# Optimization experiments

Hardware: AMD Instinct MI355X
Metric: run time of the kernel (lower is better)

The kernel has to match this reference:

```python
import jax, jax.numpy as jnp
import numpy as np

NUM_NODES = 100000
NUM_EDGES = 400000
F_IN = 16          # num_node_features
F_EDGE = 8         # num_edge_features
EMB = 16           # emb_size
NUM_GRAPHS = 256


def setup_inputs() -> dict:
    key = jax.random.key(0)
    ks = jax.random.split(key, 12)
    x = jax.random.normal(ks[0], (NUM_NODES, F_IN), dtype=jnp.float32)
    edge_index = jax.random.randint(ks[1], (2, NUM_EDGES), 0, NUM_NODES, dtype=jnp.int32)
    edge_attr = jax.random.normal(ks[2], (NUM_EDGES, F_EDGE), dtype=jnp.float32)
    batch = jnp.sort(jax.random.randint(ks[3], (NUM_NODES,), 0, NUM_GRAPHS, dtype=jnp.int32))
    s = 0.1
    # edge-network MLP: Linear(F_EDGE -> F_IN*EMB) + ReLU (torch Linear convention: W[out,in])
    nn1_w = jax.random.normal(ks[4], (F_IN * EMB, F_EDGE), dtype=jnp.float32) * s
    nn1_b = jax.random.normal(ks[5], (F_IN * EMB,), dtype=jnp.float32) * s
    # NNConv root weight (bias=False Linear) + separate bias
    root_w = jax.random.normal(ks[6], (EMB, F_IN), dtype=jnp.float32) * s
    conv_b = jax.random.normal(ks[7], (EMB,), dtype=jnp.float32) * s
    lin1_w = jax.random.normal(ks[8], (EMB, 2 * EMB), dtype=jnp.float32) * s
    lin1_b = jax.random.normal(ks[9], (EMB,), dtype=jnp.float32) * s
    lin2_w = jax.random.normal(ks[10], (1, EMB), dtype=jnp.float32) * s
    lin2_b = jax.random.normal(ks[11], (1,), dtype=jnp.float32) * s
    return {"x": x, "edge_index": edge_index, "edge_attr": edge_attr, "batch": batch,
            "nn1_w": nn1_w, "nn1_b": nn1_b, "root_w": root_w, "conv_b": conv_b,
            "lin1_w": lin1_w, "lin1_b": lin1_b, "lin2_w": lin2_w, "lin2_b": lin2_b}


def reference(x, edge_index, edge_attr, batch, nn1_w, nn1_b, root_w, conv_b,
              lin1_w, lin1_b, lin2_w, lin2_b):
    N = x.shape[0]
    src, dst = edge_index[0], edge_index[1]  # PyG: message flows src(j) -> dst(i)
    # edge network -> per-edge weight matrices [E, F_IN, EMB]
    w = jax.nn.relu(edge_attr @ nn1_w.T + nn1_b).reshape(-1, F_IN, EMB)
    # gather source features, per-edge matmul
    msg = jnp.einsum('ei,eio->eo', x[src], w)  # [E, EMB]
    # scatter-mean into target nodes
    sums = jax.ops.segment_sum(msg, dst, num_segments=N)
    cnt = jax.ops.segment_sum(jnp.ones((msg.shape[0],), msg.dtype), dst, num_segments=N)
    agg = sums / jnp.maximum(cnt, 1.0)[:, None]
    # NNConv: root transform + aggregated messages + bias, then outer ReLU
    h = jax.nn.relu(agg + x @ root_w.T + conv_b)  # [N, EMB]
    # global max pool and global mean pool per graph
    gmax = jax.ops.segment_max(h, batch, num_segments=NUM_GRAPHS)
    gsum = jax.ops.segment_sum(h, batch, num_segments=NUM_GRAPHS)
    gcnt = jax.ops.segment_sum(jnp.ones((N,), h.dtype), batch, num_segments=NUM_GRAPHS)
    gmean = gsum / jnp.maximum(gcnt, 1.0)[:, None]
    pooled = jnp.concatenate([gmax, gmean], axis=1)  # [G, 2*EMB]
    h2 = jax.nn.relu(pooled @ lin1_w.T + lin1_b)
    out = h2 @ lin2_w.T + lin2_b  # [G, 1]
    return out
```

## Files before the change

kernel.cpp:

```cpp
#include <hip/hip_runtime.h>

#define NUM_NODES 100000
#define NUM_EDGES 400000
#define F_IN 16
#define F_EDGE 8
#define EMB 16
#define NUM_GRAPHS 256

#define EDGE_GRID 2048
#define NTILES (NUM_EDGES / 64)

#define NPB 128
#define NODE_BLOCKS ((NUM_NODES + NPB - 1) / NPB)

#define WS_ZERO_FLOATS (NUM_NODES * EMB + NUM_NODES + 2 * NUM_GRAPHS * EMB + NUM_GRAPHS)

__global__ __launch_bounds__(256) void zero_kernel(float4* __restrict__ ws)
{
    const int n4 = WS_ZERO_FLOATS / 4;
    const int stride = gridDim.x * 256;
    for (int i = blockIdx.x * 256 + threadIdx.x; i < n4; i += stride)
        ws[i] = make_float4(0.f, 0.f, 0.f, 0.f);
}

__global__ __launch_bounds__(256) void edge_kernel(
    const float* __restrict__ x, const int* __restrict__ ei,
    const float* __restrict__ ea, const float* __restrict__ nn1_w,
    const float* __restrict__ nn1_b, float* __restrict__ sums,
    float* __restrict__ cnt)
{
    __shared__ float wtp[256 * 12];

    const int tid = threadIdx.x;
    const int eL  = tid >> 4;
    const int o   = tid & 15;

    #pragma unroll
    for (int t = tid; t < F_IN * EMB * F_EDGE; t += 256)
        wtp[(t >> 3) * 12 + (t & 7)] = nn1_w[t];
    wtp[tid * 12 + 8] = nn1_b[tid];
    __syncthreads();

    float br[F_IN];
    #pragma unroll
    for (int i = 0; i < F_IN; i++) br[i] = wtp[(i * 16 + o) * 12 + 8];

    for (int t = blockIdx.x; t < NTILES; t += EDGE_GRID) {
        const int e0 = t * 64 + eL * 4;

        const int4 s4 = *(const int4*)&ei[e0];
        const int4 d4 = *(const int4*)&ei[NUM_EDGES + e0];
        const int src[4] = {s4.x, s4.y, s4.z, s4.w};
        const int dst[4] = {d4.x, d4.y, d4.z, d4.w};

        float4 A[8];
        #pragma unroll
        for (int r = 0; r < 8; r++) A[r] = *(const float4*)&ea[e0 * 8 + 4 * r];

        float acc[4] = {0.f, 0.f, 0.f, 0.f};

        #pragma unroll
        for (int h = 0; h < 2; h++) {
            float4 xa[4], xb[4];
            #pragma unroll
            for (int e = 0; e < 4; e++) {
                xa[e] = *(const float4*)&x[src[e] * 16 + h * 8];
                xb[e] = *(const float4*)&x[src[e] * 16 + h * 8 + 4];
            }
            #pragma unroll
            for (int ii = 0; ii < 8; ii++) {
                const int i = h * 8 + ii;
                const float* wr = &wtp[(i * 16 + o) * 12];
                const float4 w0 = *(const float4*)wr;
                const float4 w1 = *(const float4*)(wr + 4);
                #pragma unroll
                for (int e = 0; e < 4; e++) {
                    const float4 a0 = A[2 * e];
                    const float4 a1 = A[2 * e + 1];
                    float u = br[i];
                    u = fmaf(a0.x, w0.x, u); u = fmaf(a0.y, w0.y, u);
                    u = fmaf(a0.z, w0.z, u); u = fmaf(a0.w, w0.w, u);
                    u = fmaf(a1.x, w1.x, u); u = fmaf(a1.y, w1.y, u);
                    u = fmaf(a1.z, w1.z, u); u = fmaf(a1.w, w1.w, u);
                    const float xv = (ii < 4)
                        ? ((ii == 0) ? xa[e].x : (ii == 1) ? xa[e].y
                                     : (ii == 2) ? xa[e].z : xa[e].w)
                        : ((ii == 4) ? xb[e].x : (ii == 5) ? xb[e].y
                                     : (ii == 6) ? xb[e].z : xb[e].w);
                    acc[e] = fmaf(xv, fmaxf(u, 0.f), acc[e]);
                }
            }
        }

        #pragma unroll
        for (int e = 0; e < 4; e++)
            atomicAdd(&sums[dst[e] * 16 + o], acc[e]);
        if (o == 0) {
            #pragma unroll
            for (int e = 0; e < 4; e++)
                atomicAdd(&cnt[dst[e]], 1.f);
        }
    }
}

__global__ __launch_bounds__(256) void node_kernel(
    const float* __restrict__ x, const int* __restrict__ batch,
    const float* __restrict__ root_w, const float* __restrict__ conv_b,
    const float* __restrict__ sums, const float* __restrict__ cnt,
    unsigned int* __restrict__ gmax, float* __restrict__ gsum,
    float* __restrict__ gcnt)
{
    __shared__ float rwT[256];
    __shared__ float xsh[256];
    __shared__ float ssh[256];
    __shared__ float csh[16];
    __shared__ int   bsh[16];
    __shared__ float hsh[256];

    const int tid = threadIdx.x;
    const int j   = tid >> 4;
    const int o   = tid & 15;
    const int n0  = blockIdx.x * NPB;

    rwT[(tid & 15) * 16 + (tid >> 4)] = root_w[tid];
    const float cb = conv_b[o];

    int   curg = batch[n0];
    float am = 0.f, asum = 0.f, ac = 0.f;

    for (int s0 = 0; s0 < NPB; s0 += 16) {
        const int base = n0 + s0;
        const int idx  = base * 16 + tid;
        const bool v   = (idx < NUM_NODES * 16);
        const float xv = v ? x[idx]    : 0.f;
        const float sv = v ? sums[idx] : 0.f;
        float cv = 1.f; int bv = -1;
        if (tid < 16) {
            const int n = base + tid;
            if (n < NUM_NODES) { cv = cnt[n]; bv = batch[n]; }
        }
        __syncthreads();
        xsh[tid] = xv; ssh[tid] = sv;
        if (tid < 16) { csh[tid] = cv; bsh[tid] = bv; }
        __syncthreads();

        float a = cb + ssh[j * 16 + o] / fmaxf(csh[j], 1.f);
        #pragma unroll
        for (int i = 0; i < F_IN; i++)
            a = fmaf(xsh[j * 16 + i], rwT[i * 16 + o], a);
        hsh[tid] = fmaxf(a, 0.f);
        __syncthreads();

        if (tid < 16) {
            #pragma unroll 1
            for (int jj = 0; jj < 16; jj++) {
                const int g = bsh[jj];
                if (g < 0) break;
                if (g != curg) {
                    atomicMax(&gmax[curg * 16 + o], __float_as_uint(am));
                    atomicAdd(&gsum[curg * 16 + o], asum);
                    if (o == 0) atomicAdd(&gcnt[curg], ac);
                    am = 0.f; asum = 0.f; ac = 0.f; curg = g;
                }
                const float h = hsh[jj * 16 + o];
                am = fmaxf(am, h); asum += h; ac += 1.f;
            }
        }
    }

    if (tid < 16) {
        atomicMax(&gmax[curg * 16 + o], __float_as_uint(am));
        atomicAdd(&gsum[curg * 16 + o], asum);
        if (o == 0) atomicAdd(&gcnt[curg], ac);
    }
}

__global__ __launch_bounds__(256) void head_kernel(
    const unsigned int* __restrict__ gmax, const float* __restrict__ gsum,
    const float* __restrict__ gcnt,
    const float* __restrict__ lin1_w, const float* __restrict__ lin1_b,
    const float* __restrict__ lin2_w, const float* __restrict__ lin2_b,
    float* __restrict__ out)
{
    const int g = threadIdx.x;

    float pooled[2 * EMB];
    #pragma unroll
    for (int o = 0; o < EMB; o++) pooled[o] = __uint_as_float(gmax[g * 16 + o]);
    const float c = fmaxf(gcnt[g], 1.f);
    #pragma unroll
    for (int o = 0; o < EMB; o++) pooled[EMB + o] = gsum[g * 16 + o] / c;

    float acc = lin2_b[0];
    #pragma unroll
    for (int k = 0; k < EMB; k++) {
        float a = lin1_b[k];
        #pragma unroll
        for (int cc = 0; cc < 2 * EMB; cc++)
            a = fmaf(pooled[cc], lin1_w[k * 32 + cc], a);
        acc = fmaf(fmaxf(a, 0.f), lin2_w[k], acc);
    }
    out[g] = acc;
}

extern "C" void kernel_launch(void* const* d_in, const int* in_sizes, int n_in,
                              void* d_out, int out_size, void* d_ws, size_t ws_size,
                              hipStream_t stream) {
    const float* x      = (const float*)d_in[0];
    const int*   ei     = (const int*)d_in[1];
    const float* ea     = (const float*)d_in[2];
    const int*   batch  = (const int*)d_in[3];
    const float* nn1_w  = (const float*)d_in[4];
    const float* nn1_b  = (const float*)d_in[5];
    const float* root_w = (const float*)d_in[6];
    const float* conv_b = (const float*)d_in[7];
    const float* lin1_w = (const float*)d_in[8];
    const float* lin1_b = (const float*)d_in[9];
    const float* lin2_w = (const float*)d_in[10];
    const float* lin2_b = (const float*)d_in[11];
    float* out = (float*)d_out;

    float*        sums = (float*)d_ws;
    float*        cnt  = sums + (size_t)NUM_NODES * EMB;
    unsigned int* gmax = (unsigned int*)(cnt + NUM_NODES);
    float*        gsum = (float*)(gmax + NUM_GRAPHS * EMB);
    float*        gcnt = gsum + NUM_GRAPHS * EMB;

    zero_kernel<<<1024, 256, 0, stream>>>((float4*)d_ws);
    edge_kernel<<<EDGE_GRID, 256, 0, stream>>>(x, ei, ea, nn1_w, nn1_b, sums, cnt);
    node_kernel<<<NODE_BLOCKS, 256, 0, stream>>>(
        x, batch, root_w, conv_b, sums, cnt, gmax, gsum, gcnt);
    head_kernel<<<1, 256, 0, stream>>>(gmax, gsum, gcnt,
                                       lin1_w, lin1_b, lin2_w, lin2_b, out);
}
```

Baseline: 170.3 us.

## Replace float atomic scatter with CSR bucketing via degree histogram and scan

Computes per-destination degrees with an integer histogram, builds row pointers with a multi-kernel prefix scan, and has the edge kernel write each message into a slot claimed with one integer atomic per edge. The node kernel then gathers and sums each node's messages directly instead of reading atomically accumulated sums. This removes sixteen float atomics per edge and the zeroing of the large sums buffer. In exchange it adds four extra kernel launches, a scattered message write, and divergent variable-length gather loops.

Result: slower. 205.8 us (+20.8%).

```diff
diff --git a/kernel.cpp b/kernel.cpp
--- a/kernel.cpp
+++ b/kernel.cpp
@@ -1,33 +1,96 @@
 #include <hip/hip_runtime.h>
 
-#define NUM_NODES 100000
-#define NUM_EDGES 400000
+#define NN 100000
+#define NE 400000
 #define F_IN 16
 #define F_EDGE 8
 #define EMB 16
 #define NUM_GRAPHS 256
 
 #define EDGE_GRID 2048
-#define NTILES (NUM_EDGES / 64)
+#define NTILES (NE / 64)
 
 #define NPB 128
-#define NODE_BLOCKS ((NUM_NODES + NPB - 1) / NPB)
-
-#define WS_ZERO_FLOATS (NUM_NODES * EMB + NUM_NODES + 2 * NUM_GRAPHS * EMB + NUM_GRAPHS)
-
-__global__ __launch_bounds__(256) void zero_kernel(float4* __restrict__ ws)
-{
-    const int n4 = WS_ZERO_FLOATS / 4;
-    const int stride = gridDim.x * 256;
-    for (int i = blockIdx.x * 256 + threadIdx.x; i < n4; i += stride)
-        ws[i] = make_float4(0.f, 0.f, 0.f, 0.f);
+#define NODE_BLOCKS ((NN + NPB - 1) / NPB)
+
+#define SCAN_BD 1024
+#define NSB ((NN + SCAN_BD - 1) / SCAN_BD)
+
+#define DEG_F4  (NN / 4)
+#define POOL_F4 ((2 * NUM_GRAPHS * EMB + NUM_GRAPHS) / 4)
+#define ZERO_F4 (DEG_F4 + POOL_F4)
+
+__global__ __launch_bounds__(256) void zero_kernel(float4* __restrict__ deg4,
+                                                   float4* __restrict__ pool4)
+{
+    const int i = blockIdx.x * 256 + threadIdx.x;
+    const float4 z = make_float4(0.f, 0.f, 0.f, 0.f);
+    if (i < DEG_F4) deg4[i] = z;
+    else if (i < ZERO_F4) pool4[i - DEG_F4] = z;
+}
+
+__global__ __launch_bounds__(256) void hist_kernel(const int* __restrict__ ei,
+                                                   int* __restrict__ deg)
+{
+    const int e = blockIdx.x * 256 + threadIdx.x;
+    if (e < NE) atomicAdd(&deg[ei[NE + e]], 1);
+}
+
+__global__ __launch_bounds__(SCAN_BD) void scan_blocks(const int* __restrict__ deg,
+                                                       int* __restrict__ rowptr,
+                                                       int* __restrict__ bsum)
+{
+    __shared__ int sh[SCAN_BD];
+    const int t = threadIdx.x;
+    const int i = blockIdx.x * SCAN_BD + t;
+    const int v = (i < NN) ? deg[i] : 0;
+    sh[t] = v;
+    __syncthreads();
+    #pragma unroll
+    for (int off = 1; off < SCAN_BD; off <<= 1) {
+        const int add = (t >= off) ? sh[t - off] : 0;
+        __syncthreads();
+        sh[t] += add;
+        __syncthreads();
+    }
+    if (i < NN) rowptr[i] = sh[t] - v;
+    if (t == SCAN_BD - 1) bsum[blockIdx.x] = sh[t];
+}
+
+__global__ __launch_bounds__(128) void scan_tops(int* __restrict__ bsum)
+{
+    __shared__ int sb[128];
+    const int t = threadIdx.x;
+    const int v = (t < NSB) ? bsum[t] : 0;
+    sb[t] = v;
+    __syncthreads();
+    #pragma unroll
+    for (int off = 1; off < 128; off <<= 1) {
+        const int add = (t >= off) ? sb[t - off] : 0;
+        __syncthreads();
+        sb[t] += add;
+        __syncthreads();
+    }
+    if (t < NSB) bsum[t] = sb[t] - v;
+}
+
+__global__ __launch_bounds__(SCAN_BD) void scan_add(int* __restrict__ rowptr,
+                                                    int* __restrict__ wptr,
+                                                    const int* __restrict__ bsum)
+{
+    const int i = blockIdx.x * SCAN_BD + threadIdx.x;
+    if (i < NN) {
+        const int r = rowptr[i] + bsum[blockIdx.x];
+        rowptr[i] = r;
+        wptr[i]   = r;
+    }
 }
 
 __global__ __launch_bounds__(256) void edge_kernel(
     const float* __restrict__ x, const int* __restrict__ ei,
     const float* __restrict__ ea, const float* __restrict__ nn1_w,
-    const float* __restrict__ nn1_b, float* __restrict__ sums,
-    float* __restrict__ cnt)
+    const float* __restrict__ nn1_b, int* __restrict__ wptr,
+    float* __restrict__ msg)
 {
     __shared__ float wtp[256 * 12];
 
@@ -49,7 +112,7 @@
         const int e0 = t * 64 + eL * 4;
 
         const int4 s4 = *(const int4*)&ei[e0];
-        const int4 d4 = *(const int4*)&ei[NUM_EDGES + e0];
+        const int4 d4 = *(const int4*)&ei[NE + e0];
         const int src[4] = {s4.x, s4.y, s4.z, s4.w};
         const int dst[4] = {d4.x, d4.y, d4.z, d4.w};
 
@@ -92,28 +155,30 @@
             }
         }
 
-        #pragma unroll
-        for (int e = 0; e < 4; e++)
-            atomicAdd(&sums[dst[e] * 16 + o], acc[e]);
+        int p[4] = {0, 0, 0, 0};
         if (o == 0) {
             #pragma unroll
-            for (int e = 0; e < 4; e++)
-                atomicAdd(&cnt[dst[e]], 1.f);
+            for (int e = 0; e < 4; e++) p[e] = atomicAdd(&wptr[dst[e]], 1);
         }
+        const int lb = tid & 48;
+        #pragma unroll
+        for (int e = 0; e < 4; e++) p[e] = __shfl(p[e], lb);
+        #pragma unroll
+        for (int e = 0; e < 4; e++)
+            msg[p[e] * 16 + o] = acc[e];
     }
 }
 
 __global__ __launch_bounds__(256) void node_kernel(
     const float* __restrict__ x, const int* __restrict__ batch,
     const float* __restrict__ root_w, const float* __restrict__ conv_b,
-    const float* __restrict__ sums, const float* __restrict__ cnt,
+    const int* __restrict__ rowptr, const int* __restrict__ deg,
+    const float* __restrict__ msg,
     unsigned int* __restrict__ gmax, float* __restrict__ gsum,
     float* __restrict__ gcnt)
 {
     __shared__ float rwT[256];
     __shared__ float xsh[256];
-    __shared__ float ssh[256];
-    __shared__ float csh[16];
     __shared__ int   bsh[16];
     __shared__ float hsh[256];
 
@@ -131,20 +196,22 @@
     for (int s0 = 0; s0 < NPB; s0 += 16) {
         const int base = n0 + s0;
         const int idx  = base * 16 + tid;
-        const bool v   = (idx < NUM_NODES * 16);
-        const float xv = v ? x[idx]    : 0.f;
-        const float sv = v ? sums[idx] : 0.f;
-        float cv = 1.f; int bv = -1;
-        if (tid < 16) {
-            const int n = base + tid;
-            if (n < NUM_NODES) { cv = cnt[n]; bv = batch[n]; }
-        }
-        __syncthreads();
-        xsh[tid] = xv; ssh[tid] = sv;
-        if (tid < 16) { csh[tid] = cv; bsh[tid] = bv; }
-        __syncthreads();
-
-        float a = cb + ssh[j * 16 + o] / fmaxf(csh[j], 1.f);
+        const float xv = (idx < NN * 16) ? x[idx] : 0.f;
+        const int n = base + j;
+        int st = 0, dg = 0;
+        if (n < NN) { st = rowptr[n]; dg = deg[n]; }
+        int bv = -1;
+        if (tid < 16 && base + tid < NN) bv = batch[base + tid];
+
+        __syncthreads();
+        xsh[tid] = xv;
+        if (tid < 16) bsh[tid] = bv;
+        __syncthreads();
+
+        float s = 0.f;
+        for (int k = 0; k < dg; k++) s += msg[(st + k) * 16 + o];
+
+        float a = cb + s / fmaxf((float)dg, 1.f);
         #pragma unroll
         for (int i = 0; i < F_IN; i++)
             a = fmaf(xsh[j * 16 + i], rwT[i * 16 + o], a);
@@ -220,16 +287,24 @@
     const float* lin2_b = (const float*)d_in[11];
     float* out = (float*)d_out;
 
-    float*        sums = (float*)d_ws;
-    float*        cnt  = sums + (size_t)NUM_NODES * EMB;
-    unsigned int* gmax = (unsigned int*)(cnt + NUM_NODES);
-    float*        gsum = (float*)(gmax + NUM_GRAPHS * EMB);
-    float*        gcnt = gsum + NUM_GRAPHS * EMB;
-
-    zero_kernel<<<1024, 256, 0, stream>>>((float4*)d_ws);
-    edge_kernel<<<EDGE_GRID, 256, 0, stream>>>(x, ei, ea, nn1_w, nn1_b, sums, cnt);
+    int*          deg    = (int*)d_ws;
+    int*          rowptr = deg + NN;
+    int*          wptr   = rowptr + NN;
+    int*          bsum   = wptr + NN;
+    unsigned int* gmax   = (unsigned int*)(bsum + 128);
+    float*        gsum   = (float*)(gmax + NUM_GRAPHS * EMB);
+    float*        gcnt   = gsum + NUM_GRAPHS * EMB;
+    float*        msg    = gcnt + NUM_GRAPHS;
+
+    zero_kernel<<<(ZERO_F4 + 255) / 256, 256, 0, stream>>>(
+        (float4*)deg, (float4*)gmax);
+    hist_kernel<<<(NE + 255) / 256, 256, 0, stream>>>(ei, deg);
+    scan_blocks<<<NSB, SCAN_BD, 0, stream>>>(deg, rowptr, bsum);
+    scan_tops<<<1, 128, 0, stream>>>(bsum);
+    scan_add<<<NSB, SCAN_BD, 0, stream>>>(rowptr, wptr, bsum);
+    edge_kernel<<<EDGE_GRID, 256, 0, stream>>>(x, ei, ea, nn1_w, nn1_b, wptr, msg);
     node_kernel<<<NODE_BLOCKS, 256, 0, stream>>>(
-        x, batch, root_w, conv_b, sums, cnt, gmax, gsum, gcnt);
+        x, batch, root_w, conv_b, rowptr, deg, msg, gmax, gsum, gcnt);
     head_kernel<<<1, 256, 0, stream>>>(gmax, gsum, gcnt,
                                        lin1_w, lin1_b, lin2_w, lin2_b, out);
 }
```
